# Kernel optimization log

Hardware: AMD Instinct MI355X
Metric: run time of the kernel (lower is better)

The kernel has to match this reference:

```python
import math
import jax, jax.numpy as jnp
import numpy as np

HEAD_DIM = 128
N_HEADS = 16
N_KV_HEADS = 16
LAYER_IDX = 12
LAMBDA_INIT = 0.8 - 0.6 * math.exp(-0.3 * (LAYER_IDX - 1))
EPS = 1e-5


def setup_inputs() -> dict:
    key = jax.random.key(0)
    ks = jax.random.split(key, 8)
    b, s = 2, 2048
    return {
        "q": jax.random.normal(ks[0], (b, s, N_HEADS, HEAD_DIM), jnp.float32),
        "k": jax.random.normal(ks[1], (b, s, N_KV_HEADS, HEAD_DIM), jnp.float32),
        "v": jax.random.normal(ks[2], (b, s, N_KV_HEADS, HEAD_DIM), jnp.float32),
        "lambda_q1": 0.1 * jax.random.normal(ks[3], (HEAD_DIM,), jnp.float32),
        "lambda_k1": 0.1 * jax.random.normal(ks[4], (HEAD_DIM,), jnp.float32),
        "lambda_q2": 0.1 * jax.random.normal(ks[5], (HEAD_DIM,), jnp.float32),
        "lambda_k2": 0.1 * jax.random.normal(ks[6], (HEAD_DIM,), jnp.float32),
        "subln_weight": jnp.ones((2 * HEAD_DIM,), jnp.float32),
        "attention_mask": jnp.ones((b, s), dtype=bool),
    }


def _diff_attention(q, k, v, lambda_q1, lambda_k1, lambda_q2, lambda_k2,
                    subln_weight, attention_mask):
    b, s, h, d = q.shape
    # split V into two halves along kv-head pairs, then expand back to k heads
    v5 = v.reshape(b, s, N_KV_HEADS // 2, 2, d)
    v1 = jnp.repeat(v5[..., 0, :], 2, axis=2)  # [b, s, n_kv, d]
    v2 = jnp.repeat(v5[..., 1, :], 2, axis=2)

    scale = 1.0 / math.sqrt(d)
    scores = jnp.einsum("bqhd,bkhd->bhqk", q, k) * scale
    causal = jnp.tril(jnp.ones((s, s), dtype=bool))
    pad_ok = attention_mask[:, None, None, :]  # [b,1,1,k]
    scores = jnp.where(causal[None, None] & pad_ok, scores,
                       jnp.finfo(scores.dtype).min)
    p = jax.nn.softmax(scores, axis=-1)  # shared softmax for both V halves

    attn1 = jnp.einsum("bhqk,bkhd->bqhd", p, v1)
    attn2 = jnp.einsum("bhqk,bkhd->bqhd", p, v2)

    # pair adjacent query heads: [b, s, h//2, 2, d]
    a1 = attn1.reshape(b, s, h // 2, 2, d)
    a2 = attn2.reshape(b, s, h // 2, 2, d)
    attn_1 = jnp.concatenate([a1[..., 0, :], a2[..., 0, :]], axis=-1)  # [b,s,h/2,2d]
    attn_2 = jnp.concatenate([a1[..., 1, :], a2[..., 1, :]], axis=-1)

    lam1 = jnp.exp(jnp.sum(lambda_q1 * lambda_k1))
    lam2 = jnp.exp(jnp.sum(lambda_q2 * lambda_k2))
    lambda_full = lam1 - lam2 + LAMBDA_INIT

    out = attn_1 - lambda_full * attn_2
    # RMSNorm over 2*head_dim
    rms = jax.lax.rsqrt(jnp.mean(out * out, axis=-1, keepdims=True) + EPS)
    out = out * rms * subln_weight
    return out * (1.0 - LAMBDA_INIT)


def reference(q, k, v, lambda_q1, lambda_k1, lambda_q2, lambda_k2,
              subln_weight, attention_mask):
    return _diff_attention(q, k, v, lambda_q1, lambda_k1, lambda_q2,
                           lambda_k2, subln_weight, attention_mask)
```

## Files before the change

### kernel.cpp

```cpp
#include <hip/hip_runtime.h>
#include <math.h>

namespace {
constexpr int SEQ = 2048;
constexpr int NH  = 16;
constexpr int DH  = 128;
constexpr int QB  = 64;
constexpr int KBT = 32;

typedef float f32x4 __attribute__((ext_vector_type(4)));
typedef short s16x8 __attribute__((ext_vector_type(8)));
typedef short s16x4 __attribute__((ext_vector_type(4)));
typedef unsigned short u16;

__device__ __forceinline__ u16 f2bf(float f) {
  unsigned u = __builtin_bit_cast(unsigned, f);
  return (u16)((u + 0x7fffu + ((u >> 16) & 1u)) >> 16);
}
__device__ __forceinline__ void gload16(const void* g, void* l) {
  __builtin_amdgcn_global_load_lds((const __attribute__((address_space(1))) void*)g,
                                   (__attribute__((address_space(3))) void*)l, 16, 0, 0);
}
}

__global__ __launch_bounds__(256) void prep_kernel(
    const float* __restrict__ kgl, const float* __restrict__ vg,
    u16* __restrict__ kb16, u16* __restrict__ vt16)
{
  __shared__ u16 vlds[64][132];
  const int tid = threadIdx.x, bid = blockIdx.x;
  const int kt = bid & 31, head = (bid >> 5) & 15, b = bid >> 9;
  const int k0 = kt * 64, hp = head >> 1, hh = head & 1;
  const float* ksrc = kgl + (((long)b*SEQ + k0)*NH + head)*DH;
  const float* vsrc = vg  + (((long)b*SEQ + k0)*NH + head)*DH;
  u16* kdst = kb16 + (((long)((b*8+hp)*2 + hh)*SEQ) + k0)*DH;
  #pragma unroll
  for (int i = 0; i < 8; ++i) {
    const int idx = tid + i*256, row = idx >> 5, c4 = idx & 31;
    const float4 v = *(const float4*)(ksrc + (long)row*(NH*DH) + c4*4);
    ushort4 pk = { f2bf(v.x), f2bf(v.y), f2bf(v.z), f2bf(v.w) };
    *(ushort4*)(kdst + row*DH + c4*4) = pk;
    const float4 w = *(const float4*)(vsrc + (long)row*(NH*DH) + c4*4);
    ushort4 pw = { f2bf(w.x), f2bf(w.y), f2bf(w.z), f2bf(w.w) };
    *(ushort4*)(&vlds[row][c4*4]) = pw;
  }
  __syncthreads();
  const int c = tid >> 1, half = tid & 1;
  u16* vdst = vt16 + (((long)(b*8+hp)*256) + hh*128 + c)*SEQ + k0 + half*32;
  #pragma unroll
  for (int j = 0; j < 8; ++j) {
    const int kb0 = (j >> 1)*4 + (j & 1)*16;
    ushort4 pk = { vlds[half*32 + kb0 + 0][c], vlds[half*32 + kb0 + 1][c],
                   vlds[half*32 + kb0 + 2][c], vlds[half*32 + kb0 + 3][c] };
    *(ushort4*)(vdst + j*4) = pk;
  }
}

__global__ __launch_bounds__(256, 2) void diffattn_kernel(
    const float* __restrict__ qg,
    const u16* __restrict__ kb16, const u16* __restrict__ vt16,
    const float* __restrict__ lq1, const float* __restrict__ lk1,
    const float* __restrict__ lq2, const float* __restrict__ lk2,
    const float* __restrict__ wsub, const int* __restrict__ amask,
    float* __restrict__ outp, float lambda_init)
{
  __shared__ __align__(16) unsigned char smem[65536];
  const int tid = threadIdx.x, lane = tid & 63, wid = tid >> 6;
  const int h = wid >> 1, qw = wid & 1, lr = lane & 15, kb = lane >> 4;
  const int bid = blockIdx.x;
  const int hp = bid & 7, b = (bid >> 3) & 1, p = bid >> 4;
  const int qtile = (p < 16) ? (31 - p) : (p - 16);
  const int q0 = qtile * QB;

  float s1 = lq1[lane]*lk1[lane] + lq1[lane+64]*lk1[lane+64];
  float s2 = lq2[lane]*lk2[lane] + lq2[lane+64]*lk2[lane+64];
  #pragma unroll
  for (int o = 32; o; o >>= 1) { s1 += __shfl_xor(s1, o); s2 += __shfl_xor(s2, o); }
  const float lambda_full = expf(s1) - expf(s2) + lambda_init;

  int koff[4], voff[4];
  #pragma unroll
  for (int i = 0; i < 4; ++i) {
    const int cid = tid + i*256;
    { const int hh = cid >> 9, row = (cid >> 4) & 31, ch = cid & 15;
      koff[i] = (hh*SEQ + row)*DH + (ch ^ (row & 7))*8; }
    { const int R = cid >> 4, ch = cid & 15;
      const int c = R*4 + (ch >> 2), sl = (ch & 3) ^ (R & 3);
      voff[i] = c*SEQ + sl*8; }
  }
  const u16* kbB = kb16 + (long)(b*8+hp)*2*SEQ*DH;
  const u16* vtB = vt16 + (long)(b*8+hp)*256*SEQ;

  const float qscale = 1.44269504088896f / sqrtf((float)DH);
  s16x8 qf[2][4];
  #pragma unroll
  for (int qs = 0; qs < 2; ++qs) {
    const int qrow = q0 + qw*32 + qs*16 + lr;
    const float* qp = qg + (((long)b*SEQ + qrow)*NH + hp*2 + h)*DH;
    #pragma unroll
    for (int ds = 0; ds < 4; ++ds) {
      const float4 a0 = *(const float4*)(qp + ds*32 + kb*8);
      const float4 a1 = *(const float4*)(qp + ds*32 + kb*8 + 4);
      s16x8 f;
      f[0]=(short)f2bf(a0.x*qscale); f[1]=(short)f2bf(a0.y*qscale);
      f[2]=(short)f2bf(a0.z*qscale); f[3]=(short)f2bf(a0.w*qscale);
      f[4]=(short)f2bf(a1.x*qscale); f[5]=(short)f2bf(a1.y*qscale);
      f[6]=(short)f2bf(a1.z*qscale); f[7]=(short)f2bf(a1.w*qscale);
      qf[qs][ds] = f;
    }
  }

  f32x4 acc[2][16];
  #pragma unroll
  for (int qs = 0; qs < 2; ++qs)
    #pragma unroll
    for (int i = 0; i < 16; ++i) acc[qs][i] = (f32x4){0.f,0.f,0.f,0.f};
  float m_run[2] = {-3.0e38f, -3.0e38f}, l_run[2] = {0.f, 0.f};
  const int nt = 2 * (qtile + 1);

  auto STAGE = [&](int k0s, int s) {
    unsigned char* dK = smem + s*32768;
    unsigned char* dV = dK + 16384;
    const u16* ksrc = kbB + (long)k0s*DH;
    const u16* vsrc = vtB + k0s;
    #pragma unroll
    for (int i = 0; i < 4; ++i) {
      gload16(ksrc + koff[i], dK + (tid + i*256)*16);
      gload16(vsrc + voff[i], dV + (tid + i*256)*16);
    }
  };

  STAGE(0, 0);
  __syncthreads();

  const int vofL = ((lr >> 2) << 8) + ((lr & 3) << 6) + ((kb ^ (lr >> 2)) << 4);
  const int swk = (lr & 7) << 4;

  for (int t = 0; t < nt; ++t) {
    const int cur = t & 1;
    if (t + 1 < nt) STAGE((t+1)*KBT, cur ^ 1);
    const int k0 = t * KBT;

    const int mi = amask[b*SEQ + k0 + (lane & 31)];
    const unsigned bm32 = (unsigned)__ballot(mi != 0 && lane < 32);

    const unsigned char* Kc = smem + cur*32768 + h*8192;
    s16x8 kfr[2][4];
    #pragma unroll
    for (int kt2 = 0; kt2 < 2; ++kt2) {
      const unsigned char* kr = Kc + (kt2*16 + lr)*256;
      #pragma unroll
      for (int ds = 0; ds < 4; ++ds)
        kfr[kt2][ds] = *(const s16x8*)(kr + ((ds*64 + kb*16) ^ swk));
    }

    f32x4 st[2][2];
    #pragma unroll
    for (int qs = 0; qs < 2; ++qs)
      #pragma unroll
      for (int kt2 = 0; kt2 < 2; ++kt2) {
        f32x4 c = {0.f,0.f,0.f,0.f};
        #pragma unroll
        for (int ds = 0; ds < 4; ++ds)
          c = __builtin_amdgcn_mfma_f32_16x16x32_bf16(kfr[kt2][ds], qf[qs][ds], c, 0, 0, 0);
        st[qs][kt2] = c;
      }

    float fac[2], pp[2][2][4];
    #pragma unroll
    for (int qs = 0; qs < 2; ++qs) {
      const int qmin = q0 + qw*32 + qs*16;
      const int qgrow = qmin + lr;
      const bool needmask = !((k0 + KBT - 1 <= qmin) && (bm32 == 0xffffffffu));
      float mx = -3.0e38f;
      #pragma unroll
      for (int kt2 = 0; kt2 < 2; ++kt2)
        #pragma unroll
        for (int r = 0; r < 4; ++r) {
          float sv = st[qs][kt2][r];
          if (needmask) {
            const int klo = kt2*16 + kb*4 + r;
            const bool ok = (k0 + klo <= qgrow) && ((bm32 >> klo) & 1u);
            sv = ok ? sv : -3.0e38f;
            st[qs][kt2][r] = sv;
          }
          mx = fmaxf(mx, sv);
        }
      mx = fmaxf(mx, __shfl_xor(mx, 16));
      mx = fmaxf(mx, __shfl_xor(mx, 32));
      const float mnew = fmaxf(m_run[qs], mx);
      fac[qs] = __builtin_amdgcn_exp2f(m_run[qs] - mnew);
      float lsum = 0.f;
      #pragma unroll
      for (int kt2 = 0; kt2 < 2; ++kt2)
        #pragma unroll
        for (int r = 0; r < 4; ++r) {
          const float pv = __builtin_amdgcn_exp2f(st[qs][kt2][r] - mnew);
          pp[qs][kt2][r] = pv; lsum += pv;
        }
      lsum += __shfl_xor(lsum, 16); lsum += __shfl_xor(lsum, 32);
      l_run[qs] = l_run[qs]*fac[qs] + lsum;
      m_run[qs] = mnew;
    }

    const bool nores = (fac[0] == 1.f) & (fac[1] == 1.f);
    if (!__all(nores)) {
      #pragma unroll
      for (int qs = 0; qs < 2; ++qs) {
        float fq[4];
        #pragma unroll
        for (int r = 0; r < 4; ++r) fq[r] = __shfl(fac[qs], kb*4 + r);
        #pragma unroll
        for (int ct = 0; ct < 16; ++ct) {
          acc[qs][ct][0]*=fq[0]; acc[qs][ct][1]*=fq[1];
          acc[qs][ct][2]*=fq[2]; acc[qs][ct][3]*=fq[3];
        }
      }
    }

    s16x4 pa[2][2];
    #pragma unroll
    for (int qs = 0; qs < 2; ++qs)
      #pragma unroll
      for (int kt2 = 0; kt2 < 2; ++kt2) {
        s16x4 tt = { (short)f2bf(pp[qs][kt2][0]), (short)f2bf(pp[qs][kt2][1]),
                     (short)f2bf(pp[qs][kt2][2]), (short)f2bf(pp[qs][kt2][3]) };
        pa[qs][kt2] = tt;
      }

    const unsigned char* Vc = smem + cur*32768 + 16384;
    #pragma unroll
    for (int ct = 0; ct < 16; ++ct) {
      const s16x8 vf = *(const s16x8*)(Vc + ct*1024 + vofL);
      const s16x4 v0 = { vf[0], vf[1], vf[2], vf[3] };
      const s16x4 v1 = { vf[4], vf[5], vf[6], vf[7] };
      #pragma unroll
      for (int qs = 0; qs < 2; ++qs) {
        acc[qs][ct] = __builtin_amdgcn_mfma_f32_16x16x16bf16_1k(pa[qs][0], v0, acc[qs][ct], 0, 0, 0);
        acc[qs][ct] = __builtin_amdgcn_mfma_f32_16x16x16bf16_1k(pa[qs][1], v1, acc[qs][ct], 0, 0, 0);
      }
    }
    __syncthreads();
  }

  float lqv[2][4];
  #pragma unroll
  for (int qs = 0; qs < 2; ++qs)
    #pragma unroll
    for (int r = 0; r < 4; ++r) lqv[qs][r] = 1.f / __shfl(l_run[qs], kb*4 + r);
  unsigned char* OB = smem + qw*32768;
  if (h == 1) {
    #pragma unroll
    for (int qs = 0; qs < 2; ++qs)
      #pragma unroll
      for (int ct = 0; ct < 16; ++ct) {
        const int c = ct*16 + lr;
        const int byteo = (qs*64 + kb*16) ^ ((c & 7) << 4);
        f32x4 v = { acc[qs][ct][0]*lqv[qs][0], acc[qs][ct][1]*lqv[qs][1],
                    acc[qs][ct][2]*lqv[qs][2], acc[qs][ct][3]*lqv[qs][3] };
        *(f32x4*)(OB + c*128 + byteo) = v;
      }
  }
  __syncthreads();
  if (h == 0) {
    float ss[2][4] = {{0.f,0.f,0.f,0.f},{0.f,0.f,0.f,0.f}};
    #pragma unroll
    for (int qs = 0; qs < 2; ++qs)
      #pragma unroll
      for (int ct = 0; ct < 16; ++ct) {
        const int c = ct*16 + lr;
        const int byteo = (qs*64 + kb*16) ^ ((c & 7) << 4);
        const f32x4 ob = *(const f32x4*)(OB + c*128 + byteo);
        #pragma unroll
        for (int r = 0; r < 4; ++r) {
          const float v = acc[qs][ct][r]*lqv[qs][r] - lambda_full*ob[r];
          acc[qs][ct][r] = v; ss[qs][r] += v*v;
        }
      }
    #pragma unroll
    for (int o = 8; o; o >>= 1)
      #pragma unroll
      for (int qs = 0; qs < 2; ++qs)
        #pragma unroll
        for (int r = 0; r < 4; ++r) ss[qs][r] += __shfl_xor(ss[qs][r], o);
    const float fin = 1.f - lambda_init;
    float rms[2][4];
    #pragma unroll
    for (int qs = 0; qs < 2; ++qs)
      #pragma unroll
      for (int r = 0; r < 4; ++r)
        rms[qs][r] = rsqrtf(ss[qs][r]*(1.f/256.f) + 1e-5f) * fin;
    #pragma unroll
    for (int qs = 0; qs < 2; ++qs)
      #pragma unroll
      for (int ct = 0; ct < 16; ++ct) {
        const int c = ct*16 + lr;
        const float wv = wsub[c];
        #pragma unroll
        for (int r = 0; r < 4; ++r) {
          const long q = q0 + qw*32 + qs*16 + kb*4 + r;
          outp[(((long)b*SEQ + q)*8 + hp)*256 + c] = acc[qs][ct][r]*rms[qs][r]*wv;
        }
      }
  }
}

extern "C" void kernel_launch(void* const* d_in, const int* in_sizes, int n_in,
                              void* d_out, int out_size, void* d_ws, size_t ws_size,
                              hipStream_t stream) {
  (void)in_sizes; (void)n_in; (void)out_size; (void)ws_size;
  const float lambda_init = (float)(0.8 - 0.6 * exp(-0.3 * (12 - 1)));
  u16* kb16 = (u16*)d_ws;
  u16* vt16 = (u16*)((char*)d_ws + (size_t)16*1024*1024);
  prep_kernel<<<dim3(1024), dim3(256), 0, stream>>>(
      (const float*)d_in[1], (const float*)d_in[2], kb16, vt16);
  diffattn_kernel<<<dim3(512), dim3(256), 0, stream>>>(
      (const float*)d_in[0], kb16, vt16,
      (const float*)d_in[3], (const float*)d_in[4], (const float*)d_in[5],
      (const float*)d_in[6], (const float*)d_in[7],
      (const int*)d_in[8],
      (float*)d_out, lambda_init);
}
```

Baseline: 297.3 us.

## Double K tile to 64 and pair causal q-tiles per block for load balance

The key tile grows from 32 to 64 rows, so each iteration stages twice as much K/V into a 128 KB LDS buffer and runs more MFMAs per barrier. Each block now processes two query tiles (p and 31-p) in sequence, which balances causal work across 256 blocks instead of launching 512 blocks with uneven lengths. The intent is to amortise barriers and per-tile overhead and to even out per-block work. In exchange occupancy falls to one block per CU, with 256 blocks on a 256-CU device, so there is less latency hiding and less tail flexibility.

```diff
diff --git a/kernel.cpp b/kernel.cpp
--- a/kernel.cpp
+++ b/kernel.cpp
@@ -6,7 +6,7 @@
 constexpr int NH  = 16;
 constexpr int DH  = 128;
 constexpr int QB  = 64;
-constexpr int KBT = 32;
+constexpr int KBT = 64;
 
 typedef float f32x4 __attribute__((ext_vector_type(4)));
 typedef short s16x8 __attribute__((ext_vector_type(8)));
@@ -56,7 +56,7 @@
   }
 }
 
-__global__ __launch_bounds__(256, 2) void diffattn_kernel(
+__global__ __launch_bounds__(256, 1) void diffattn_kernel(
     const float* __restrict__ qg,
     const u16* __restrict__ kb16, const u16* __restrict__ vt16,
     const float* __restrict__ lq1, const float* __restrict__ lk1,
@@ -64,13 +64,11 @@
     const float* __restrict__ wsub, const int* __restrict__ amask,
     float* __restrict__ outp, float lambda_init)
 {
-  __shared__ __align__(16) unsigned char smem[65536];
+  __shared__ __align__(16) unsigned char smem[131072];
   const int tid = threadIdx.x, lane = tid & 63, wid = tid >> 6;
   const int h = wid >> 1, qw = wid & 1, lr = lane & 15, kb = lane >> 4;
   const int bid = blockIdx.x;
   const int hp = bid & 7, b = (bid >> 3) & 1, p = bid >> 4;
-  const int qtile = (p < 16) ? (31 - p) : (p - 16);
-  const int q0 = qtile * QB;
 
   float s1 = lq1[lane]*lk1[lane] + lq1[lane+64]*lk1[lane+64];
   float s2 = lq2[lane]*lk2[lane] + lq2[lane+64]*lk2[lane+64];
@@ -78,230 +76,233 @@
   for (int o = 32; o; o >>= 1) { s1 += __shfl_xor(s1, o); s2 += __shfl_xor(s2, o); }
   const float lambda_full = expf(s1) - expf(s2) + lambda_init;
 
-  int koff[4], voff[4];
+  int koff[8], voff[8];
   #pragma unroll
-  for (int i = 0; i < 4; ++i) {
+  for (int i = 0; i < 8; ++i) {
     const int cid = tid + i*256;
-    { const int hh = cid >> 9, row = (cid >> 4) & 31, ch = cid & 15;
+    { const int hh = cid >> 10, row = (cid >> 4) & 63, ch = cid & 15;
       koff[i] = (hh*SEQ + row)*DH + (ch ^ (row & 7))*8; }
-    { const int R = cid >> 4, ch = cid & 15;
-      const int c = R*4 + (ch >> 2), sl = (ch & 3) ^ (R & 3);
-      voff[i] = c*SEQ + sl*8; }
+    { const int R = cid >> 5, ch = cid & 31;
+      const int c = R*4 + ((ch >> 2) & 3), khalf = ch >> 4, sl = (ch & 3) ^ (R & 3);
+      voff[i] = c*SEQ + khalf*32 + sl*8; }
   }
   const u16* kbB = kb16 + (long)(b*8+hp)*2*SEQ*DH;
   const u16* vtB = vt16 + (long)(b*8+hp)*256*SEQ;
 
-  const float qscale = 1.44269504088896f / sqrtf((float)DH);
-  s16x8 qf[2][4];
-  #pragma unroll
-  for (int qs = 0; qs < 2; ++qs) {
-    const int qrow = q0 + qw*32 + qs*16 + lr;
-    const float* qp = qg + (((long)b*SEQ + qrow)*NH + hp*2 + h)*DH;
-    #pragma unroll
-    for (int ds = 0; ds < 4; ++ds) {
-      const float4 a0 = *(const float4*)(qp + ds*32 + kb*8);
-      const float4 a1 = *(const float4*)(qp + ds*32 + kb*8 + 4);
-      s16x8 f;
-      f[0]=(short)f2bf(a0.x*qscale); f[1]=(short)f2bf(a0.y*qscale);
-      f[2]=(short)f2bf(a0.z*qscale); f[3]=(short)f2bf(a0.w*qscale);
-      f[4]=(short)f2bf(a1.x*qscale); f[5]=(short)f2bf(a1.y*qscale);
-      f[6]=(short)f2bf(a1.z*qscale); f[7]=(short)f2bf(a1.w*qscale);
-      qf[qs][ds] = f;
-    }
-  }
-
-  f32x4 acc[2][16];
-  #pragma unroll
-  for (int qs = 0; qs < 2; ++qs)
-    #pragma unroll
-    for (int i = 0; i < 16; ++i) acc[qs][i] = (f32x4){0.f,0.f,0.f,0.f};
-  float m_run[2] = {-3.0e38f, -3.0e38f}, l_run[2] = {0.f, 0.f};
-  const int nt = 2 * (qtile + 1);
-
   auto STAGE = [&](int k0s, int s) {
-    unsigned char* dK = smem + s*32768;
-    unsigned char* dV = dK + 16384;
+    unsigned char* dK = smem + s*65536;
+    unsigned char* dV = dK + 32768;
     const u16* ksrc = kbB + (long)k0s*DH;
     const u16* vsrc = vtB + k0s;
     #pragma unroll
-    for (int i = 0; i < 4; ++i) {
+    for (int i = 0; i < 8; ++i) {
       gload16(ksrc + koff[i], dK + (tid + i*256)*16);
       gload16(vsrc + voff[i], dV + (tid + i*256)*16);
     }
   };
 
-  STAGE(0, 0);
-  __syncthreads();
-
-  const int vofL = ((lr >> 2) << 8) + ((lr & 3) << 6) + ((kb ^ (lr >> 2)) << 4);
+  const float qscale = 1.44269504088896f / sqrtf((float)DH);
+  const int vof0 = ((lr >> 2) << 9) + ((lr & 3) << 6) + ((kb ^ (lr >> 2)) << 4);
   const int swk = (lr & 7) << 4;
 
-  for (int t = 0; t < nt; ++t) {
-    const int cur = t & 1;
-    if (t + 1 < nt) STAGE((t+1)*KBT, cur ^ 1);
-    const int k0 = t * KBT;
-
-    const int mi = amask[b*SEQ + k0 + (lane & 31)];
-    const unsigned bm32 = (unsigned)__ballot(mi != 0 && lane < 32);
-
-    const unsigned char* Kc = smem + cur*32768 + h*8192;
-    s16x8 kfr[2][4];
+  #pragma unroll 1
+  for (int qi = 0; qi < 2; ++qi) {
+    const int qtile = qi ? (31 - p) : p;
+    const int q0 = qtile * QB;
+    __syncthreads();
+
+    s16x8 qf[2][4];
     #pragma unroll
-    for (int kt2 = 0; kt2 < 2; ++kt2) {
-      const unsigned char* kr = Kc + (kt2*16 + lr)*256;
-      #pragma unroll
-      for (int ds = 0; ds < 4; ++ds)
-        kfr[kt2][ds] = *(const s16x8*)(kr + ((ds*64 + kb*16) ^ swk));
-    }
-
-    f32x4 st[2][2];
+    for (int qs = 0; qs < 2; ++qs) {
+      const int qrow = q0 + qw*32 + qs*16 + lr;
+      const float* qp = qg + (((long)b*SEQ + qrow)*NH + hp*2 + h)*DH;
+      #pragma unroll
+      for (int ds = 0; ds < 4; ++ds) {
+        const float4 a0 = *(const float4*)(qp + ds*32 + kb*8);
+        const float4 a1 = *(const float4*)(qp + ds*32 + kb*8 + 4);
+        s16x8 f;
+        f[0]=(short)f2bf(a0.x*qscale); f[1]=(short)f2bf(a0.y*qscale);
+        f[2]=(short)f2bf(a0.z*qscale); f[3]=(short)f2bf(a0.w*qscale);
+        f[4]=(short)f2bf(a1.x*qscale); f[5]=(short)f2bf(a1.y*qscale);
+        f[6]=(short)f2bf(a1.z*qscale); f[7]=(short)f2bf(a1.w*qscale);
+        qf[qs][ds] = f;
+      }
+    }
+
+    f32x4 acc[2][16];
     #pragma unroll
     for (int qs = 0; qs < 2; ++qs)
       #pragma unroll
-      for (int kt2 = 0; kt2 < 2; ++kt2) {
-        f32x4 c = {0.f,0.f,0.f,0.f};
-        #pragma unroll
-        for (int ds = 0; ds < 4; ++ds)
-          c = __builtin_amdgcn_mfma_f32_16x16x32_bf16(kfr[kt2][ds], qf[qs][ds], c, 0, 0, 0);
-        st[qs][kt2] = c;
-      }
-
-    float fac[2], pp[2][2][4];
-    #pragma unroll
-    for (int qs = 0; qs < 2; ++qs) {
-      const int qmin = q0 + qw*32 + qs*16;
-      const int qgrow = qmin + lr;
-      const bool needmask = !((k0 + KBT - 1 <= qmin) && (bm32 == 0xffffffffu));
-      float mx = -3.0e38f;
-      #pragma unroll
-      for (int kt2 = 0; kt2 < 2; ++kt2)
-        #pragma unroll
-        for (int r = 0; r < 4; ++r) {
-          float sv = st[qs][kt2][r];
-          if (needmask) {
-            const int klo = kt2*16 + kb*4 + r;
-            const bool ok = (k0 + klo <= qgrow) && ((bm32 >> klo) & 1u);
-            sv = ok ? sv : -3.0e38f;
-            st[qs][kt2][r] = sv;
-          }
-          mx = fmaxf(mx, sv);
-        }
-      mx = fmaxf(mx, __shfl_xor(mx, 16));
-      mx = fmaxf(mx, __shfl_xor(mx, 32));
-      const float mnew = fmaxf(m_run[qs], mx);
-      fac[qs] = __builtin_amdgcn_exp2f(m_run[qs] - mnew);
-      float lsum = 0.f;
-      #pragma unroll
-      for (int kt2 = 0; kt2 < 2; ++kt2)
-        #pragma unroll
-        for (int r = 0; r < 4; ++r) {
-          const float pv = __builtin_amdgcn_exp2f(st[qs][kt2][r] - mnew);
-          pp[qs][kt2][r] = pv; lsum += pv;
-        }
-      lsum += __shfl_xor(lsum, 16); lsum += __shfl_xor(lsum, 32);
-      l_run[qs] = l_run[qs]*fac[qs] + lsum;
-      m_run[qs] = mnew;
-    }
-
-    const bool nores = (fac[0] == 1.f) & (fac[1] == 1.f);
-    if (!__all(nores)) {
+      for (int i = 0; i < 16; ++i) acc[qs][i] = (f32x4){0.f,0.f,0.f,0.f};
+    float m_run[2] = {-3.0e38f, -3.0e38f}, l_run[2] = {0.f, 0.f};
+    const int nt = qtile + 1;
+
+    STAGE(0, 0);
+    __syncthreads();
+
+    for (int t = 0; t < nt; ++t) {
+      const int cur = t & 1;
+      if (t + 1 < nt) STAGE((t+1)*KBT, cur ^ 1);
+      const int k0 = t * KBT;
+
+      const int mi = amask[b*SEQ + k0 + lane];
+      const unsigned long long bm64 = __ballot(mi != 0);
+
+      const unsigned char* Kc = smem + cur*65536 + h*16384;
+      f32x4 st[2][4];
+      #pragma unroll
+      for (int kt2 = 0; kt2 < 4; ++kt2) {
+        const unsigned char* kr = Kc + (kt2*16 + lr)*256;
+        f32x4 c0 = {0.f,0.f,0.f,0.f}, c1 = {0.f,0.f,0.f,0.f};
+        #pragma unroll
+        for (int ds = 0; ds < 4; ++ds) {
+          const s16x8 af = *(const s16x8*)(kr + ((ds*64 + kb*16) ^ swk));
+          c0 = __builtin_amdgcn_mfma_f32_16x16x32_bf16(af, qf[0][ds], c0, 0, 0, 0);
+          c1 = __builtin_amdgcn_mfma_f32_16x16x32_bf16(af, qf[1][ds], c1, 0, 0, 0);
+        }
+        st[0][kt2] = c0; st[1][kt2] = c1;
+      }
+
+      float fac[2], pp[2][4][4];
       #pragma unroll
       for (int qs = 0; qs < 2; ++qs) {
-        float fq[4];
-        #pragma unroll
-        for (int r = 0; r < 4; ++r) fq[r] = __shfl(fac[qs], kb*4 + r);
-        #pragma unroll
-        for (int ct = 0; ct < 16; ++ct) {
-          acc[qs][ct][0]*=fq[0]; acc[qs][ct][1]*=fq[1];
-          acc[qs][ct][2]*=fq[2]; acc[qs][ct][3]*=fq[3];
-        }
-      }
-    }
-
-    s16x4 pa[2][2];
+        const int qmin = q0 + qw*32 + qs*16;
+        const int qgrow = qmin + lr;
+        const bool needmask = !((k0 + KBT - 1 <= qmin) && (bm64 == ~0ull));
+        float mx = -3.0e38f;
+        #pragma unroll
+        for (int kt2 = 0; kt2 < 4; ++kt2)
+          #pragma unroll
+          for (int r = 0; r < 4; ++r) {
+            float sv = st[qs][kt2][r];
+            if (needmask) {
+              const int klo = kt2*16 + kb*4 + r;
+              const bool ok = (k0 + klo <= qgrow) && ((bm64 >> klo) & 1ull);
+              sv = ok ? sv : -3.0e38f;
+              st[qs][kt2][r] = sv;
+            }
+            mx = fmaxf(mx, sv);
+          }
+        mx = fmaxf(mx, __shfl_xor(mx, 16));
+        mx = fmaxf(mx, __shfl_xor(mx, 32));
+        const float mnew = fmaxf(m_run[qs], mx);
+        fac[qs] = __builtin_amdgcn_exp2f(m_run[qs] - mnew);
+        float lsum = 0.f;
+        #pragma unroll
+        for (int kt2 = 0; kt2 < 4; ++kt2)
+          #pragma unroll
+          for (int r = 0; r < 4; ++r) {
+            const float pv = __builtin_amdgcn_exp2f(st[qs][kt2][r] - mnew);
+            pp[qs][kt2][r] = pv; lsum += pv;
+          }
+        lsum += __shfl_xor(lsum, 16); lsum += __shfl_xor(lsum, 32);
+        l_run[qs] = l_run[qs]*fac[qs] + lsum;
+        m_run[qs] = mnew;
+      }
+
+      const bool nores = (fac[0] == 1.f) & (fac[1] == 1.f);
+      if (!__all(nores)) {
+        #pragma unroll
+        for (int qs = 0; qs < 2; ++qs) {
+          float fq[4];
+          #pragma unroll
+          for (int r = 0; r < 4; ++r) fq[r] = __shfl(fac[qs], kb*4 + r);
+          #pragma unroll
+          for (int ct = 0; ct < 16; ++ct) {
+            acc[qs][ct][0]*=fq[0]; acc[qs][ct][1]*=fq[1];
+            acc[qs][ct][2]*=fq[2]; acc[qs][ct][3]*=fq[3];
+          }
+        }
+      }
+
+      s16x4 pa[2][4];
+      #pragma unroll
+      for (int qs = 0; qs < 2; ++qs)
+        #pragma unroll
+        for (int kt2 = 0; kt2 < 4; ++kt2) {
+          s16x4 tt = { (short)f2bf(pp[qs][kt2][0]), (short)f2bf(pp[qs][kt2][1]),
+                       (short)f2bf(pp[qs][kt2][2]), (short)f2bf(pp[qs][kt2][3]) };
+          pa[qs][kt2] = tt;
+        }
+
+      const unsigned char* Vc = smem + cur*65536 + 32768;
+      #pragma unroll
+      for (int ct = 0; ct < 16; ++ct) {
+        #pragma unroll
+        for (int khalf = 0; khalf < 2; ++khalf) {
+          const s16x8 vf = *(const s16x8*)(Vc + ct*2048 + vof0 + khalf*256);
+          const s16x4 v0 = { vf[0], vf[1], vf[2], vf[3] };
+          const s16x4 v1 = { vf[4], vf[5], vf[6], vf[7] };
+          #pragma unroll
+          for (int qs = 0; qs < 2; ++qs) {
+            acc[qs][ct] = __builtin_amdgcn_mfma_f32_16x16x16bf16_1k(pa[qs][khalf*2+0], v0, acc[qs][ct], 0, 0, 0);
+            acc[qs][ct] = __builtin_amdgcn_mfma_f32_16x16x16bf16_1k(pa[qs][khalf*2+1], v1, acc[qs][ct], 0, 0, 0);
+          }
+        }
+      }
+      __syncthreads();
+    }
+
+    float lqv[2][4];
     #pragma unroll
     for (int qs = 0; qs < 2; ++qs)
       #pragma unroll
-      for (int kt2 = 0; kt2 < 2; ++kt2) {
-        s16x4 tt = { (short)f2bf(pp[qs][kt2][0]), (short)f2bf(pp[qs][kt2][1]),
-                     (short)f2bf(pp[qs][kt2][2]), (short)f2bf(pp[qs][kt2][3]) };
-        pa[qs][kt2] = tt;
-      }
-
-    const unsigned char* Vc = smem + cur*32768 + 16384;
-    #pragma unroll
-    for (int ct = 0; ct < 16; ++ct) {
-      const s16x8 vf = *(const s16x8*)(Vc + ct*1024 + vofL);
-      const s16x4 v0 = { vf[0], vf[1], vf[2], vf[3] };
-      const s16x4 v1 = { vf[4], vf[5], vf[6], vf[7] };
-      #pragma unroll
-      for (int qs = 0; qs < 2; ++qs) {
-        acc[qs][ct] = __builtin_amdgcn_mfma_f32_16x16x16bf16_1k(pa[qs][0], v0, acc[qs][ct], 0, 0, 0);
-        acc[qs][ct] = __builtin_amdgcn_mfma_f32_16x16x16bf16_1k(pa[qs][1], v1, acc[qs][ct], 0, 0, 0);
-      }
+      for (int r = 0; r < 4; ++r) lqv[qs][r] = 1.f / __shfl(l_run[qs], kb*4 + r);
+    unsigned char* OB = smem + qw*32768;
+    if (h == 1) {
+      #pragma unroll
+      for (int qs = 0; qs < 2; ++qs)
+        #pragma unroll
+        for (int ct = 0; ct < 16; ++ct) {
+          const int c = ct*16 + lr;
+          const int byteo = (qs*64 + kb*16) ^ ((c & 7) << 4);
+          f32x4 v = { acc[qs][ct][0]*lqv[qs][0], acc[qs][ct][1]*lqv[qs][1],
+                      acc[qs][ct][2]*lqv[qs][2], acc[qs][ct][3]*lqv[qs][3] };
+          *(f32x4*)(OB + c*128 + byteo) = v;
+        }
     }
     __syncthreads();
-  }
-
-  float lqv[2][4];
-  #pragma unroll
-  for (int qs = 0; qs < 2; ++qs)
-    #pragma unroll
-    for (int r = 0; r < 4; ++r) lqv[qs][r] = 1.f / __shfl(l_run[qs], kb*4 + r);
-  unsigned char* OB = smem + qw*32768;
-  if (h == 1) {
-    #pragma unroll
-    for (int qs = 0; qs < 2; ++qs)
-      #pragma unroll
-      for (int ct = 0; ct < 16; ++ct) {
-        const int c = ct*16 + lr;
-        const int byteo = (qs*64 + kb*16) ^ ((c & 7) << 4);
-        f32x4 v = { acc[qs][ct][0]*lqv[qs][0], acc[qs][ct][1]*lqv[qs][1],
-                    acc[qs][ct][2]*lqv[qs][2], acc[qs][ct][3]*lqv[qs][3] };
-        *(f32x4*)(OB + c*128 + byteo) = v;
-      }
-  }
-  __syncthreads();
-  if (h == 0) {
-    float ss[2][4] = {{0.f,0.f,0.f,0.f},{0.f,0.f,0.f,0.f}};
-    #pragma unroll
-    for (int qs = 0; qs < 2; ++qs)
-      #pragma unroll
-      for (int ct = 0; ct < 16; ++ct) {
-        const int c = ct*16 + lr;
-        const int byteo = (qs*64 + kb*16) ^ ((c & 7) << 4);
-        const f32x4 ob = *(const f32x4*)(OB + c*128 + byteo);
-        #pragma unroll
-        for (int r = 0; r < 4; ++r) {
-          const float v = acc[qs][ct][r]*lqv[qs][r] - lambda_full*ob[r];
-          acc[qs][ct][r] = v; ss[qs][r] += v*v;
-        }
-      }
-    #pragma unroll
-    for (int o = 8; o; o >>= 1)
-      #pragma unroll
-      for (int qs = 0; qs < 2; ++qs)
-        #pragma unroll
-        for (int r = 0; r < 4; ++r) ss[qs][r] += __shfl_xor(ss[qs][r], o);
-    const float fin = 1.f - lambda_init;
-    float rms[2][4];
-    #pragma unroll
-    for (int qs = 0; qs < 2; ++qs)
-      #pragma unroll
-      for (int r = 0; r < 4; ++r)
-        rms[qs][r] = rsqrtf(ss[qs][r]*(1.f/256.f) + 1e-5f) * fin;
-    #pragma unroll
-    for (int qs = 0; qs < 2; ++qs)
-      #pragma unroll
-      for (int ct = 0; ct < 16; ++ct) {
-        const int c = ct*16 + lr;
-        const float wv = wsub[c];
-        #pragma unroll
-        for (int r = 0; r < 4; ++r) {
-          const long q = q0 + qw*32 + qs*16 + kb*4 + r;
-          outp[(((long)b*SEQ + q)*8 + hp)*256 + c] = acc[qs][ct][r]*rms[qs][r]*wv;
-        }
-      }
+    if (h == 0) {
+      float ss[2][4] = {{0.f,0.f,0.f,0.f},{0.f,0.f,0.f,0.f}};
+      #pragma unroll
+      for (int qs = 0; qs < 2; ++qs)
+        #pragma unroll
+        for (int ct = 0; ct < 16; ++ct) {
+          const int c = ct*16 + lr;
+          const int byteo = (qs*64 + kb*16) ^ ((c & 7) << 4);
+          const f32x4 ob = *(const f32x4*)(OB + c*128 + byteo);
+          #pragma unroll
+          for (int r = 0; r < 4; ++r) {
+            const float v = acc[qs][ct][r]*lqv[qs][r] - lambda_full*ob[r];
+            acc[qs][ct][r] = v; ss[qs][r] += v*v;
+          }
+        }
+      #pragma unroll
+      for (int o = 8; o; o >>= 1)
+        #pragma unroll
+        for (int qs = 0; qs < 2; ++qs)
+          #pragma unroll
+          for (int r = 0; r < 4; ++r) ss[qs][r] += __shfl_xor(ss[qs][r], o);
+      const float fin = 1.f - lambda_init;
+      float rms[2][4];
+      #pragma unroll
+      for (int qs = 0; qs < 2; ++qs)
+        #pragma unroll
+        for (int r = 0; r < 4; ++r)
+          rms[qs][r] = rsqrtf(ss[qs][r]*(1.f/256.f) + 1e-5f) * fin;
+      #pragma unroll
+      for (int qs = 0; qs < 2; ++qs)
+        #pragma unroll
+        for (int ct = 0; ct < 16; ++ct) {
+          const int c = ct*16 + lr;
+          const float wv = wsub[c];
+          #pragma unroll
+          for (int r = 0; r < 4; ++r) {
+            const long q = q0 + qw*32 + qs*16 + kb*4 + r;
+            outp[(((long)b*SEQ + q)*8 + hp)*256 + c] = acc[qs][ct][r]*rms[qs][r]*wv;
+          }
+        }
+    }
   }
 }
 
@@ -314,7 +315,7 @@
   u16* vt16 = (u16*)((char*)d_ws + (size_t)16*1024*1024);
   prep_kernel<<<dim3(1024), dim3(256), 0, stream>>>(
       (const float*)d_in[1], (const float*)d_in[2], kb16, vt16);
-  diffattn_kernel<<<dim3(512), dim3(256), 0, stream>>>(
+  diffattn_kernel<<<dim3(256), dim3(256), 0, stream>>>(
       (const float*)d_in[0], kb16, vt16,
       (const float*)d_in[3], (const float*)d_in[4], (const float*)d_in[5],
       (const float*)d_in[6], (const float*)d_in[7],
```

New measurement: 320.7 us. +7.9%, slower.
